# Kernel optimization log

Hardware: AMD Instinct MI355X
Metric: run time of the kernel (lower is better)

## Reference

```python
import jax, jax.numpy as jnp
import numpy as np

N_NODES = 100000
N_EDGES = 800000
IN_FEAT = 128
HID = 128
OUT = 2


def setup_inputs() -> dict:
    key = jax.random.key(0)
    ks = jax.random.split(key, 8)
    h = jax.random.normal(ks[0], (N_NODES, IN_FEAT), dtype=jnp.float32)
    src = jax.random.randint(ks[1], (N_EDGES,), 0, N_NODES, dtype=jnp.int64)
    dst = jax.random.randint(ks[2], (N_EDGES,), 0, N_NODES, dtype=jnp.int64)
    # Linear weights stored as (fan_in, fan_out); scaled like torch's default init
    W1 = jax.random.normal(ks[3], (2 * IN_FEAT, HID), dtype=jnp.float32) / np.sqrt(2 * IN_FEAT)
    b1 = jnp.zeros((HID,), dtype=jnp.float32)
    W2 = jax.random.normal(ks[4], (HID, HID), dtype=jnp.float32) / np.sqrt(HID)
    b2 = jnp.zeros((HID,), dtype=jnp.float32)
    W3 = jax.random.normal(ks[5], (HID, OUT), dtype=jnp.float32) / np.sqrt(HID)
    b3 = jnp.zeros((OUT,), dtype=jnp.float32)
    return {"h": h, "src": src, "dst": dst,
            "W1": W1, "b1": b1, "W2": W2, "b2": b2, "W3": W3, "b3": b3}


def reference(h, src, dst, W1, b1, W2, b2, W3, b3):
    # Per-edge gather of endpoint features, concat, 3-layer MLP with ReLU
    h_u = h[src]                       # [E, F]
    h_v = h[dst]                       # [E, F]
    x = jnp.concatenate([h_u, h_v], axis=1)   # [E, 2F]
    x = jax.nn.relu(x @ W1 + b1)       # [E, HID]
    x = jax.nn.relu(x @ W2 + b2)       # [E, HID]
    score = x @ W3 + b3                # [E, OUT]
    return score
```

## Files before the change

### kernel.cpp

```cpp
#include <hip/hip_runtime.h>
#include <hip/hip_fp16.h>


typedef _Float16 half8 __attribute__((ext_vector_type(8)));
typedef float    f32x4 __attribute__((ext_vector_type(4)));

#define N_NODES_C 100000
#define N_EDGES_C 800000
#define NT        12500
#define GRID_MAIN 512

#define W1F_OFF   0
#define W2F_OFF   65536
#define W3F_OFF   98304
#define H16_OFF   131072
#define H16_BYTES (N_NODES_C * 128 * 2)
#define WS_NEED   ((size_t)H16_OFF + (size_t)H16_BYTES)

#define MFMA16(a, b, c) __builtin_amdgcn_mfma_f32_16x16x32_f16((a), (b), (c), 0, 0, 0)


__global__ void conv_h_kernel(const float* __restrict__ h, _Float16* __restrict__ h16, int n8) {
    int stride = gridDim.x * blockDim.x;
    for (int i = blockIdx.x * blockDim.x + threadIdx.x; i < n8; i += stride) {
        const float4* p = (const float4*)h + 2 * (size_t)i;
        float4 a = p[0], b = p[1];
        half8 o;
        o[0] = (_Float16)a.x; o[1] = (_Float16)a.y; o[2] = (_Float16)a.z; o[3] = (_Float16)a.w;
        o[4] = (_Float16)b.x; o[5] = (_Float16)b.y; o[6] = (_Float16)b.z; o[7] = (_Float16)b.w;
        ((half8*)h16)[i] = o;
    }
}

__global__ void pack_w_kernel(const float* __restrict__ W1, const float* __restrict__ W2,
                              const float* __restrict__ W3, char* __restrict__ wsb) {
    int i = blockIdx.x * blockDim.x + threadIdx.x;
    _Float16* w1f = (_Float16*)(wsb + W1F_OFF);
    _Float16* w2f = (_Float16*)(wsb + W2F_OFF);
    _Float16* w3f = (_Float16*)(wsb + W3F_OFF);
    if (i < 32768) {
        int j = i & 7, lx = (i >> 3) & 63, kk = (i >> 9) & 7, t = i >> 12;
        int k = 32 * kk + 8 * (lx >> 4) + j, n = 16 * t + (lx & 15);
        w1f[i] = (_Float16)W1[k * 128 + n];
    }
    if (i < 16384) {
        int j = i & 7, lx = (i >> 3) & 63, kk = (i >> 9) & 3, t = i >> 11;
        int k = 32 * kk + 8 * (lx >> 4) + j, n = 16 * t + (lx & 15);
        w2f[i] = (_Float16)W2[k * 128 + n];
    }
    if (i < 2048) {
        int j = i & 7, lx = (i >> 3) & 63, kk = i >> 9;
        int k = 32 * kk + 8 * (lx >> 4) + j, n = lx & 15;
        w3f[i] = (n < 2) ? (_Float16)W3[k * 2 + n] : (_Float16)0.0f;
    }
}


template <bool USE16>
__device__ inline half8 ldfrag(const float* __restrict__ h, const half8* __restrict__ h16,
                               int idx, int kk, int g) {
    if constexpr (USE16) {
        return h16[idx * 16 + (kk & 3) * 4 + g];
    } else {
        const float4* p = (const float4*)(h + (size_t)idx * 128 + (kk & 3) * 32 + g * 8);
        float4 a = p[0], b = p[1];
        half8 o;
        o[0] = (_Float16)a.x; o[1] = (_Float16)a.y; o[2] = (_Float16)a.z; o[3] = (_Float16)a.w;
        o[4] = (_Float16)b.x; o[5] = (_Float16)b.y; o[6] = (_Float16)b.z; o[7] = (_Float16)b.w;
        return o;
    }
}

template <bool USE16>
__global__ __launch_bounds__(256, 2) void edge_mlp_kernel(
    const float* __restrict__ h,
    const int*   __restrict__ src,
    const int*   __restrict__ dst,
    const float* __restrict__ b1,
    const float* __restrict__ b2,
    const float* __restrict__ b3,
    const char*  __restrict__ wsb,
    float*       __restrict__ out) {
    __shared__ half8 Xp [32 * 64];
    __shared__ half8 Y1p[16 * 64];
    __shared__ half8 Y2p[16 * 64];

    const int tid = threadIdx.x;
    const int w = tid >> 6, l = tid & 63;
    const int g = l >> 4, rr = l & 15;
    const int ghalf = rr >> 3, j7 = rr & 7;

    half8 W1F[2][8], W2F[2][4], W3F[4];
    {
        const half8* p1 = (const half8*)(wsb + W1F_OFF);
        const half8* p2 = (const half8*)(wsb + W2F_OFF);
        const half8* p3 = (const half8*)(wsb + W3F_OFF);
#pragma unroll
        for (int nt = 0; nt < 2; ++nt)
#pragma unroll
            for (int kk = 0; kk < 8; ++kk)
                W1F[nt][kk] = p1[((w * 2 + nt) * 8 + kk) * 64 + l];
#pragma unroll
        for (int nt = 0; nt < 2; ++nt)
#pragma unroll
            for (int kk = 0; kk < 4; ++kk)
                W2F[nt][kk] = p2[((w * 2 + nt) * 4 + kk) * 64 + l];
#pragma unroll
        for (int kk = 0; kk < 4; ++kk)
            W3F[kk] = p3[kk * 64 + l];
    }
    float b1r[2], b2r[2];
    b1r[0] = b1[w * 32 + rr];      b1r[1] = b1[w * 32 + 16 + rr];
    b2r[0] = b2[w * 32 + rr];      b2r[1] = b2[w * 32 + 16 + rr];
    const float b3r = (rr < 2) ? b3[rr] : 0.0f;

    const half8* h16 = (const half8*)(wsb + H16_OFF);
    _Float16* y1h = (_Float16*)Y1p;
    _Float16* y2h = (_Float16*)Y2p;

    int   idxn[8];
    half8 xt[8];

    int tile = blockIdx.x;
#pragma unroll
    for (int i = 0; i < 8; i++) {
        int bidx = w * 8 + i, kk = bidx >> 2;
        int e = ((i & 3) << 4) + rr;
        int id = (kk < 4 ? src : dst)[tile * 64 + e];
        xt[i] = ldfrag<USE16>(h, h16, id, kk, g);
    }
#pragma unroll
    for (int i = 0; i < 8; i++) Xp[(w * 8 + i) * 64 + l] = xt[i];
    {
        int t1 = tile + GRID_MAIN; if (t1 >= NT) t1 = NT - 1;
#pragma unroll
        for (int i = 0; i < 8; i++) {
            int bidx = w * 8 + i, kk = bidx >> 2;
            int e = ((i & 3) << 4) + rr;
            idxn[i] = (kk < 4 ? src : dst)[t1 * 64 + e];
        }
    }
    __syncthreads();

    for (; tile < NT; tile += GRID_MAIN) {
        f32x4 acc1[4][2];
#pragma unroll
        for (int mt = 0; mt < 4; ++mt) {
            acc1[mt][0] = f32x4{0.f, 0.f, 0.f, 0.f};
            acc1[mt][1] = f32x4{0.f, 0.f, 0.f, 0.f};
        }
#pragma unroll
        for (int kk = 0; kk < 8; ++kk) {
            half8 a[4];
#pragma unroll
            for (int mt = 0; mt < 4; ++mt) a[mt] = Xp[(kk * 4 + mt) * 64 + l];
#pragma unroll
            for (int mt = 0; mt < 4; ++mt) {
                acc1[mt][0] = MFMA16(a[mt], W1F[0][kk], acc1[mt][0]);
                acc1[mt][1] = MFMA16(a[mt], W1F[1][kk], acc1[mt][1]);
            }
        }
#pragma unroll
        for (int i = 0; i < 8; i++) {
            int kk = (w * 8 + i) >> 2;
            xt[i] = ldfrag<USE16>(h, h16, idxn[i], kk, g);
        }
        {
            int t2 = tile + 2 * GRID_MAIN; if (t2 >= NT) t2 = NT - 1;
#pragma unroll
            for (int i = 0; i < 8; i++) {
                int bidx = w * 8 + i, kk = bidx >> 2;
                int e = ((i & 3) << 4) + rr;
                idxn[i] = (kk < 4 ? src : dst)[t2 * 64 + e];
            }
        }
#pragma unroll
        for (int mt = 0; mt < 4; ++mt)
#pragma unroll
            for (int nt = 0; nt < 2; ++nt) {
                float bb = b1r[nt];
#pragma unroll
                for (int r = 0; r < 4; ++r) {
                    float v = acc1[mt][nt][r] + bb;
                    v = v > 0.f ? v : 0.f;
                    y1h[(((w * 4 + mt) * 64 + 16 * (2 * nt + ghalf) + 4 * g + r) << 3) + j7] =
                        (_Float16)v;
                }
            }
        __syncthreads();

        f32x4 acc2[4][2];
#pragma unroll
        for (int mt = 0; mt < 4; ++mt) {
            acc2[mt][0] = f32x4{0.f, 0.f, 0.f, 0.f};
            acc2[mt][1] = f32x4{0.f, 0.f, 0.f, 0.f};
        }
#pragma unroll
        for (int kk = 0; kk < 4; ++kk) {
            half8 a[4];
#pragma unroll
            for (int mt = 0; mt < 4; ++mt) a[mt] = Y1p[(kk * 4 + mt) * 64 + l];
#pragma unroll
            for (int mt = 0; mt < 4; ++mt) {
                acc2[mt][0] = MFMA16(a[mt], W2F[0][kk], acc2[mt][0]);
                acc2[mt][1] = MFMA16(a[mt], W2F[1][kk], acc2[mt][1]);
            }
        }
#pragma unroll
        for (int mt = 0; mt < 4; ++mt)
#pragma unroll
            for (int nt = 0; nt < 2; ++nt) {
                float bb = b2r[nt];
#pragma unroll
                for (int r = 0; r < 4; ++r) {
                    float v = acc2[mt][nt][r] + bb;
                    v = v > 0.f ? v : 0.f;
                    y2h[(((w * 4 + mt) * 64 + 16 * (2 * nt + ghalf) + 4 * g + r) << 3) + j7] =
                        (_Float16)v;
                }
            }
        __syncthreads();

        f32x4 acc3 = {0.f, 0.f, 0.f, 0.f};
#pragma unroll
        for (int kk = 0; kk < 4; ++kk) {
            half8 a = Y2p[(kk * 4 + w) * 64 + l];
            acc3 = MFMA16(a, W3F[kk], acc3);
        }
        if (rr < 2) {
#pragma unroll
            for (int r = 0; r < 4; ++r) {
                int m = w * 16 + 4 * g + r;
                out[(tile * 64 + m) * 2 + rr] = acc3[r] + b3r;
            }
        }
#pragma unroll
        for (int i = 0; i < 8; i++) Xp[(w * 8 + i) * 64 + l] = xt[i];
        __syncthreads();
    }
}


extern "C" void kernel_launch(void* const* d_in, const int* in_sizes, int n_in,
                              void* d_out, int out_size, void* d_ws, size_t ws_size,
                              hipStream_t stream) {
    const float* h  = (const float*)d_in[0];
    const int*   src = (const int*)d_in[1];
    const int*   dst = (const int*)d_in[2];
    const float* W1 = (const float*)d_in[3];
    const float* b1 = (const float*)d_in[4];
    const float* W2 = (const float*)d_in[5];
    const float* b2 = (const float*)d_in[6];
    const float* W3 = (const float*)d_in[7];
    const float* b3 = (const float*)d_in[8];
    char*  wsb = (char*)d_ws;
    float* out = (float*)d_out;
    (void)in_sizes; (void)n_in; (void)out_size;

    pack_w_kernel<<<128, 256, 0, stream>>>(W1, W2, W3, wsb);
    if (ws_size >= WS_NEED) {
        conv_h_kernel<<<2048, 256, 0, stream>>>(h, (_Float16*)(wsb + H16_OFF),
                                                N_NODES_C * 128 / 8);
        edge_mlp_kernel<true><<<GRID_MAIN, 256, 0, stream>>>(h, src, dst, b1, b2, b3, wsb, out);
    } else {
        edge_mlp_kernel<false><<<GRID_MAIN, 256, 0, stream>>>(h, src, dst, b1, b2, b3, wsb, out);
    }
}
```

Measured before the change: 199.8 us.

## Precompute per-node layer-1 projections and gather them per edge

Splits the first linear layer across the concatenation so each node's features are projected once through both halves of W1 into fp16 tables, then edges gather and sum the two projections before ReLU and layers 2 and 3. This removes the per-edge layer-1 matmul, which is redundant since there are far fewer nodes than edges. The edge kernel is retiled to 32 edges per block with two waves splitting the output columns. The trade-offs are a larger workspace requirement, with a fallback to the old path if it is not met, and fp16 rounding of the pre-activation sums.

After: 249.9 us. +25.1%, slower.

```diff
diff --git a/kernel.cpp b/kernel.cpp
--- a/kernel.cpp
+++ b/kernel.cpp
@@ -3,41 +3,230 @@
 
 
 typedef _Float16 half8 __attribute__((ext_vector_type(8)));
+typedef _Float16 half4_t __attribute__((ext_vector_type(4)));
 typedef float    f32x4 __attribute__((ext_vector_type(4)));
+
+#define MFMA16(a, b, c) __builtin_amdgcn_mfma_f32_16x16x32_f16((a), (b), (c), 0, 0, 0)
 
 #define N_NODES_C 100000
 #define N_EDGES_C 800000
-#define NT        12500
-#define GRID_MAIN 512
-
-#define W1F_OFF   0
-#define W2F_OFF   65536
-#define W3F_OFF   98304
-#define H16_OFF   131072
-#define H16_BYTES (N_NODES_C * 128 * 2)
-#define WS_NEED   ((size_t)H16_OFF + (size_t)H16_BYTES)
-
-#define MFMA16(a, b, c) __builtin_amdgcn_mfma_f32_16x16x32_f16((a), (b), (c), 0, 0, 0)
-
-
-__global__ void conv_h_kernel(const float* __restrict__ h, _Float16* __restrict__ h16, int n8) {
-    int stride = gridDim.x * blockDim.x;
-    for (int i = blockIdx.x * blockDim.x + threadIdx.x; i < n8; i += stride) {
-        const float4* p = (const float4*)h + 2 * (size_t)i;
-        float4 a = p[0], b = p[1];
-        half8 o;
-        o[0] = (_Float16)a.x; o[1] = (_Float16)a.y; o[2] = (_Float16)a.z; o[3] = (_Float16)a.w;
-        o[4] = (_Float16)b.x; o[5] = (_Float16)b.y; o[6] = (_Float16)b.z; o[7] = (_Float16)b.w;
-        ((half8*)h16)[i] = o;
-    }
-}
-
-__global__ void pack_w_kernel(const float* __restrict__ W1, const float* __restrict__ W2,
-                              const float* __restrict__ W3, char* __restrict__ wsb) {
+
+#define W1PF_OFF  0
+#define W1QF_OFF  32768
+#define W2F_OFF_N 65536
+#define W3F_OFF_N 98304
+#define P16_OFF   131072
+#define TBL_HALVES (N_NODES_C * 128)
+#define Q16_OFF   (P16_OFF + TBL_HALVES * 2)
+#define WS_NEED_NEW ((size_t)Q16_OFF + (size_t)TBL_HALVES * 2)
+
+#define ET 32
+#define NT_E (N_EDGES_C / ET)
+#define GRID_E 1536
+#define NT_N ((N_NODES_C + 63) / 64)
+
+
+__global__ void pack_w_new(const float* __restrict__ W1, const float* __restrict__ W2,
+                           const float* __restrict__ W3, char* __restrict__ wsb) {
     int i = blockIdx.x * blockDim.x + threadIdx.x;
-    _Float16* w1f = (_Float16*)(wsb + W1F_OFF);
-    _Float16* w2f = (_Float16*)(wsb + W2F_OFF);
-    _Float16* w3f = (_Float16*)(wsb + W3F_OFF);
+    _Float16* w1pf = (_Float16*)(wsb + W1PF_OFF);
+    _Float16* w1qf = (_Float16*)(wsb + W1QF_OFF);
+    _Float16* w2f  = (_Float16*)(wsb + W2F_OFF_N);
+    _Float16* w3f  = (_Float16*)(wsb + W3F_OFF_N);
+    if (i < 16384) {
+        int j = i & 7, lane = (i >> 3) & 63, kk = (i >> 9) & 3, cm = i >> 11;
+        int g = lane >> 4, rr = lane & 15;
+        int k = 32 * kk + 8 * g + j, n = 16 * cm + rr;
+        w1pf[i] = (_Float16)W1[k * 128 + n];
+        w1qf[i] = (_Float16)W1[(k + 128) * 128 + n];
+        w2f[i]  = (_Float16)W2[k * 128 + n];
+    }
+    if (i < 2048) {
+        int j = i & 7, lane = (i >> 3) & 63, t = i >> 9;
+        int g = lane >> 4, rr = lane & 15;
+        int k = 32 * t + 4 * g + (j & 3) + 16 * (j >> 2);
+        w3f[i] = (rr < 2) ? (_Float16)W3[k * 2 + rr] : (_Float16)0.0f;
+    }
+}
+
+__global__ __launch_bounds__(512, 4) void pq_kernel(const float* __restrict__ h,
+                                                    const float* __restrict__ b1,
+                                                    char* __restrict__ wsb) {
+    const int tid = threadIdx.x;
+    const int w = tid >> 6, l = tid & 63, g = l >> 4, rr = l & 15;
+    const int t = w >> 2, cmq = w & 3;
+    const half8* wf = (const half8*)(wsb + (t ? W1QF_OFF : W1PF_OFF));
+    half8 W1F[2][4];
+#pragma unroll
+    for (int cm = 0; cm < 2; ++cm)
+#pragma unroll
+        for (int kk = 0; kk < 4; ++kk)
+            W1F[cm][kk] = wf[((2 * cmq + cm) * 4 + kk) * 64 + l];
+    f32x4 b1v[2] = {{0.f, 0.f, 0.f, 0.f}, {0.f, 0.f, 0.f, 0.f}};
+    if (t == 1) {
+#pragma unroll
+        for (int cm = 0; cm < 2; ++cm)
+            b1v[cm] = *(const f32x4*)(b1 + 16 * (2 * cmq + cm) + 4 * g);
+    }
+    _Float16* tbl = (_Float16*)(wsb + (t ? Q16_OFF : P16_OFF));
+
+    for (int tile = blockIdx.x; tile < NT_N; tile += gridDim.x) {
+        f32x4 acc[2][4];
+#pragma unroll
+        for (int cm = 0; cm < 2; ++cm)
+#pragma unroll
+            for (int ce = 0; ce < 4; ++ce) acc[cm][ce] = f32x4{0.f, 0.f, 0.f, 0.f};
+#pragma unroll
+        for (int kk = 0; kk < 4; ++kk) {
+#pragma unroll
+            for (int ce = 0; ce < 4; ++ce) {
+                int node = tile * 64 + 16 * ce + rr;
+                if (node > N_NODES_C - 1) node = N_NODES_C - 1;
+                const float4* hp = (const float4*)(h + (size_t)node * 128 + kk * 32 + 8 * g);
+                float4 fa = hp[0], fb = hp[1];
+                half8 b;
+                b[0] = (_Float16)fa.x; b[1] = (_Float16)fa.y;
+                b[2] = (_Float16)fa.z; b[3] = (_Float16)fa.w;
+                b[4] = (_Float16)fb.x; b[5] = (_Float16)fb.y;
+                b[6] = (_Float16)fb.z; b[7] = (_Float16)fb.w;
+                acc[0][ce] = MFMA16(W1F[0][kk], b, acc[0][ce]);
+                acc[1][ce] = MFMA16(W1F[1][kk], b, acc[1][ce]);
+            }
+        }
+#pragma unroll
+        for (int cm = 0; cm < 2; ++cm)
+#pragma unroll
+            for (int ce = 0; ce < 4; ++ce) {
+                int node = tile * 64 + 16 * ce + rr;
+                if (node < N_NODES_C) {
+                    f32x4 v = acc[cm][ce] + b1v[cm];
+                    half4_t o;
+                    o[0] = (_Float16)v[0]; o[1] = (_Float16)v[1];
+                    o[2] = (_Float16)v[2]; o[3] = (_Float16)v[3];
+                    *(half4_t*)(tbl + (size_t)node * 128 + 16 * (2 * cmq + cm) + 4 * g) = o;
+                }
+            }
+    }
+}
+
+__global__ __launch_bounds__(128, 3) void edge_kernel(
+    const int* __restrict__ src, const int* __restrict__ dst,
+    const float* __restrict__ b2, const float* __restrict__ b3,
+    const char* __restrict__ wsb, float* __restrict__ out) {
+    __shared__ float2 part[2][2][16];
+    const int tid = threadIdx.x;
+    const int w = tid >> 6, l = tid & 63, g = l >> 4, rr = l & 15;
+    const half8* w2f = (const half8*)(wsb + W2F_OFF_N);
+    const half8* w3f = (const half8*)(wsb + W3F_OFF_N);
+    const half8* P16 = (const half8*)(wsb + P16_OFF);
+    const half8* Q16 = (const half8*)(wsb + Q16_OFF);
+
+    half8 W2F[4][4], W3F[2];
+#pragma unroll
+    for (int cm = 0; cm < 4; ++cm)
+#pragma unroll
+        for (int kk = 0; kk < 4; ++kk)
+            W2F[cm][kk] = w2f[((4 * w + cm) * 4 + kk) * 64 + l];
+    W3F[0] = w3f[(2 * w) * 64 + l];
+    W3F[1] = w3f[(2 * w + 1) * 64 + l];
+
+    half4_t b2h[4];
+#pragma unroll
+    for (int cm = 0; cm < 4; ++cm) {
+        f32x4 bv = *(const f32x4*)(b2 + 16 * (4 * w + cm) + 4 * g);
+        b2h[cm][0] = (_Float16)bv[0]; b2h[cm][1] = (_Float16)bv[1];
+        b2h[cm][2] = (_Float16)bv[2]; b2h[cm][3] = (_Float16)bv[3];
+    }
+    const float b30 = b3[0], b31 = b3[1];
+
+    int tile = blockIdx.x;
+    int sc0 = src[tile * ET + rr],      sc1 = src[tile * ET + 16 + rr];
+    int dc0 = dst[tile * ET + rr],      dc1 = dst[tile * ET + 16 + rr];
+    int par = 0;
+
+    for (; tile < NT_E; tile += GRID_E) {
+        int ntile = tile + GRID_E; if (ntile >= NT_E) ntile = NT_E - 1;
+        f32x4 acc[4][2];
+#pragma unroll
+        for (int cm = 0; cm < 4; ++cm) {
+            acc[cm][0] = f32x4{0.f, 0.f, 0.f, 0.f};
+            acc[cm][1] = f32x4{0.f, 0.f, 0.f, 0.f};
+        }
+        const half8* pr0 = P16 + (size_t)sc0 * 16 + g;
+        const half8* pr1 = P16 + (size_t)sc1 * 16 + g;
+        const half8* qr0 = Q16 + (size_t)dc0 * 16 + g;
+        const half8* qr1 = Q16 + (size_t)dc1 * 16 + g;
+        const half8 hz = {0, 0, 0, 0, 0, 0, 0, 0};
+#pragma unroll
+        for (int kk = 0; kk < 4; ++kk) {
+            {
+                half8 p = pr0[4 * kk], q = qr0[4 * kk];
+                half8 b = __builtin_elementwise_max(p + q, hz);
+                acc[0][0] = MFMA16(W2F[0][kk], b, acc[0][0]);
+                acc[1][0] = MFMA16(W2F[1][kk], b, acc[1][0]);
+                acc[2][0] = MFMA16(W2F[2][kk], b, acc[2][0]);
+                acc[3][0] = MFMA16(W2F[3][kk], b, acc[3][0]);
+            }
+            {
+                half8 p = pr1[4 * kk], q = qr1[4 * kk];
+                half8 b = __builtin_elementwise_max(p + q, hz);
+                acc[0][1] = MFMA16(W2F[0][kk], b, acc[0][1]);
+                acc[1][1] = MFMA16(W2F[1][kk], b, acc[1][1]);
+                acc[2][1] = MFMA16(W2F[2][kk], b, acc[2][1]);
+                acc[3][1] = MFMA16(W2F[3][kk], b, acc[3][1]);
+            }
+        }
+        int sn0 = src[ntile * ET + rr], sn1 = src[ntile * ET + 16 + rr];
+        int dn0 = dst[ntile * ET + rr], dn1 = dst[ntile * ET + 16 + rr];
+
+        f32x4 D3[2] = {{0.f, 0.f, 0.f, 0.f}, {0.f, 0.f, 0.f, 0.f}};
+#pragma unroll
+        for (int tl = 0; tl < 2; ++tl)
+#pragma unroll
+            for (int ce = 0; ce < 2; ++ce) {
+                half8 bf;
+#pragma unroll
+                for (int j = 0; j < 8; ++j) {
+                    const int cm = 2 * tl + (j >> 2), r = j & 3;
+                    float v = acc[cm][ce][r] + (float)b2h[cm][r];
+                    v = v > 0.f ? v : 0.f;
+                    bf[j] = (_Float16)v;
+                }
+                D3[ce] = MFMA16(W3F[tl], bf, D3[ce]);
+            }
+        if (w == 1 && l < 16) {
+            part[par][0][rr] = make_float2(D3[0][0], D3[0][1]);
+            part[par][1][rr] = make_float2(D3[1][0], D3[1][1]);
+        }
+        __syncthreads();
+        if (w == 0 && l < 16) {
+#pragma unroll
+            for (int ce = 0; ce < 2; ++ce) {
+                float2 pp = part[par][ce][rr];
+                float2 ov;
+                ov.x = D3[ce][0] + pp.x + b30;
+                ov.y = D3[ce][1] + pp.y + b31;
+                *(float2*)(out + (size_t)(tile * ET + 16 * ce + rr) * 2) = ov;
+            }
+        }
+        par ^= 1;
+        sc0 = sn0; sc1 = sn1; dc0 = dn0; dc1 = dn1;
+    }
+}
+
+
+#define NT_O   12500
+#define GRID_O 512
+#define OW1_OFF 0
+#define OW2_OFF 65536
+#define OW3_OFF 98304
+
+__global__ void pack_w_old(const float* __restrict__ W1, const float* __restrict__ W2,
+                           const float* __restrict__ W3, char* __restrict__ wsb) {
+    int i = blockIdx.x * blockDim.x + threadIdx.x;
+    _Float16* w1f = (_Float16*)(wsb + OW1_OFF);
+    _Float16* w2f = (_Float16*)(wsb + OW2_OFF);
+    _Float16* w3f = (_Float16*)(wsb + OW3_OFF);
     if (i < 32768) {
         int j = i & 7, lx = (i >> 3) & 63, kk = (i >> 9) & 7, t = i >> 12;
         int k = 32 * kk + 8 * (lx >> 4) + j, n = 16 * t + (lx & 15);
@@ -55,84 +244,62 @@
     }
 }
 
-
-template <bool USE16>
-__device__ inline half8 ldfrag(const float* __restrict__ h, const half8* __restrict__ h16,
-                               int idx, int kk, int g) {
-    if constexpr (USE16) {
-        return h16[idx * 16 + (kk & 3) * 4 + g];
-    } else {
-        const float4* p = (const float4*)(h + (size_t)idx * 128 + (kk & 3) * 32 + g * 8);
-        float4 a = p[0], b = p[1];
-        half8 o;
-        o[0] = (_Float16)a.x; o[1] = (_Float16)a.y; o[2] = (_Float16)a.z; o[3] = (_Float16)a.w;
-        o[4] = (_Float16)b.x; o[5] = (_Float16)b.y; o[6] = (_Float16)b.z; o[7] = (_Float16)b.w;
-        return o;
-    }
-}
-
-template <bool USE16>
-__global__ __launch_bounds__(256, 2) void edge_mlp_kernel(
-    const float* __restrict__ h,
-    const int*   __restrict__ src,
-    const int*   __restrict__ dst,
-    const float* __restrict__ b1,
-    const float* __restrict__ b2,
-    const float* __restrict__ b3,
-    const char*  __restrict__ wsb,
-    float*       __restrict__ out) {
+__device__ inline half8 ldfrag_f32(const float* __restrict__ h, int idx, int kk, int g) {
+    const float4* p = (const float4*)(h + (size_t)idx * 128 + (kk & 3) * 32 + g * 8);
+    float4 a = p[0], b = p[1];
+    half8 o;
+    o[0] = (_Float16)a.x; o[1] = (_Float16)a.y; o[2] = (_Float16)a.z; o[3] = (_Float16)a.w;
+    o[4] = (_Float16)b.x; o[5] = (_Float16)b.y; o[6] = (_Float16)b.z; o[7] = (_Float16)b.w;
+    return o;
+}
+
+__global__ __launch_bounds__(256, 2) void edge_mlp_old(
+    const float* __restrict__ h, const int* __restrict__ src, const int* __restrict__ dst,
+    const float* __restrict__ b1, const float* __restrict__ b2, const float* __restrict__ b3,
+    const char* __restrict__ wsb, float* __restrict__ out) {
     __shared__ half8 Xp [32 * 64];
     __shared__ half8 Y1p[16 * 64];
     __shared__ half8 Y2p[16 * 64];
-
     const int tid = threadIdx.x;
     const int w = tid >> 6, l = tid & 63;
     const int g = l >> 4, rr = l & 15;
     const int ghalf = rr >> 3, j7 = rr & 7;
-
     half8 W1F[2][8], W2F[2][4], W3F[4];
     {
-        const half8* p1 = (const half8*)(wsb + W1F_OFF);
-        const half8* p2 = (const half8*)(wsb + W2F_OFF);
-        const half8* p3 = (const half8*)(wsb + W3F_OFF);
+        const half8* p1 = (const half8*)(wsb + OW1_OFF);
+        const half8* p2 = (const half8*)(wsb + OW2_OFF);
+        const half8* p3 = (const half8*)(wsb + OW3_OFF);
 #pragma unroll
         for (int nt = 0; nt < 2; ++nt)
 #pragma unroll
-            for (int kk = 0; kk < 8; ++kk)
-                W1F[nt][kk] = p1[((w * 2 + nt) * 8 + kk) * 64 + l];
+            for (int kk = 0; kk < 8; ++kk) W1F[nt][kk] = p1[((w * 2 + nt) * 8 + kk) * 64 + l];
 #pragma unroll
         for (int nt = 0; nt < 2; ++nt)
 #pragma unroll
-            for (int kk = 0; kk < 4; ++kk)
-                W2F[nt][kk] = p2[((w * 2 + nt) * 4 + kk) * 64 + l];
-#pragma unroll
-        for (int kk = 0; kk < 4; ++kk)
-            W3F[kk] = p3[kk * 64 + l];
+            for (int kk = 0; kk < 4; ++kk) W2F[nt][kk] = p2[((w * 2 + nt) * 4 + kk) * 64 + l];
+#pragma unroll
+        for (int kk = 0; kk < 4; ++kk) W3F[kk] = p3[kk * 64 + l];
     }
     float b1r[2], b2r[2];
     b1r[0] = b1[w * 32 + rr];      b1r[1] = b1[w * 32 + 16 + rr];
     b2r[0] = b2[w * 32 + rr];      b2r[1] = b2[w * 32 + 16 + rr];
     const float b3r = (rr < 2) ? b3[rr] : 0.0f;
-
-    const half8* h16 = (const half8*)(wsb + H16_OFF);
     _Float16* y1h = (_Float16*)Y1p;
     _Float16* y2h = (_Float16*)Y2p;
-
     int   idxn[8];
     half8 xt[8];
-
     int tile = blockIdx.x;
 #pragma unroll
     for (int i = 0; i < 8; i++) {
         int bidx = w * 8 + i, kk = bidx >> 2;
         int e = ((i & 3) << 4) + rr;
         int id = (kk < 4 ? src : dst)[tile * 64 + e];
-        xt[i] = ldfrag<USE16>(h, h16, id, kk, g);
+        xt[i] = ldfrag_f32(h, id, kk, g);
     }
 #pragma unroll
     for (int i = 0; i < 8; i++) Xp[(w * 8 + i) * 64 + l] = xt[i];
     {
-        int t1 = tile + GRID_MAIN; if (t1 >= NT) t1 = NT - 1;
+        int t1 = tile + GRID_O; if (t1 >= NT_O) t1 = NT_O - 1;
 #pragma unroll
         for (int i = 0; i < 8; i++) {
             int bidx = w * 8 + i, kk = bidx >> 2;
@@ -141,8 +308,7 @@
         }
     }
     __syncthreads();
-
-    for (; tile < NT; tile += GRID_MAIN) {
+    for (; tile < NT_O; tile += GRID_O) {
         f32x4 acc1[4][2];
 #pragma unroll
         for (int mt = 0; mt < 4; ++mt) {
@@ -163,10 +329,10 @@
 #pragma unroll
         for (int i = 0; i < 8; i++) {
             int kk = (w * 8 + i) >> 2;
-            xt[i] = ldfrag<USE16>(h, h16, idxn[i], kk, g);
+            xt[i] = ldfrag_f32(h, idxn[i], kk, g);
         }
         {
-            int t2 = tile + 2 * GRID_MAIN; if (t2 >= NT) t2 = NT - 1;
+            int t2 = tile + 2 * GRID_O; if (t2 >= NT_O) t2 = NT_O - 1;
 #pragma unroll
             for (int i = 0; i < 8; i++) {
                 int bidx = w * 8 + i, kk = bidx >> 2;
@@ -188,7 +354,6 @@
                 }
             }
         __syncthreads();
-
         f32x4 acc2[4][2];
 #pragma unroll
         for (int mt = 0; mt < 4; ++mt) {
@@ -220,7 +385,6 @@
                 }
             }
         __syncthreads();
-
         f32x4 acc3 = {0.f, 0.f, 0.f, 0.f};
 #pragma unroll
         for (int kk = 0; kk < 4; ++kk) {
@@ -244,25 +408,25 @@
 extern "C" void kernel_launch(void* const* d_in, const int* in_sizes, int n_in,
                               void* d_out, int out_size, void* d_ws, size_t ws_size,
                               hipStream_t stream) {
-    const float* h  = (const float*)d_in[0];
+    const float* h   = (const float*)d_in[0];
     const int*   src = (const int*)d_in[1];
     const int*   dst = (const int*)d_in[2];
-    const float* W1 = (const float*)d_in[3];
-    const float* b1 = (const float*)d_in[4];
-    const float* W2 = (const float*)d_in[5];
-    const float* b2 = (const float*)d_in[6];
-    const float* W3 = (const float*)d_in[7];
-    const float* b3 = (const float*)d_in[8];
+    const float* W1  = (const float*)d_in[3];
+    const float* b1  = (const float*)d_in[4];
+    const float* W2  = (const float*)d_in[5];
+    const float* b2  = (const float*)d_in[6];
+    const float* W3  = (const float*)d_in[7];
+    const float* b3  = (const float*)d_in[8];
     char*  wsb = (char*)d_ws;
     float* out = (float*)d_out;
     (void)in_sizes; (void)n_in; (void)out_size;
 
-    pack_w_kernel<<<128, 256, 0, stream>>>(W1, W2, W3, wsb);
-    if (ws_size >= WS_NEED) {
-        conv_h_kernel<<<2048, 256, 0, stream>>>(h, (_Float16*)(wsb + H16_OFF),
-                                                N_NODES_C * 128 / 8);
-        edge_mlp_kernel<true><<<GRID_MAIN, 256, 0, stream>>>(h, src, dst, b1, b2, b3, wsb, out);
+    if (ws_size >= WS_NEED_NEW) {
+        pack_w_new<<<64, 256, 0, stream>>>(W1, W2, W3, wsb);
+        pq_kernel<<<512, 512, 0, stream>>>(h, b1, wsb);
+        edge_kernel<<<GRID_E, 128, 0, stream>>>(src, dst, b2, b3, wsb, out);
     } else {
-        edge_mlp_kernel<false><<<GRID_MAIN, 256, 0, stream>>>(h, src, dst, b1, b2, b3, wsb, out);
-    }
-}
+        pack_w_old<<<128, 256, 0, stream>>>(W1, W2, W3, wsb);
+        edge_mlp_old<<<GRID_O, 256, 0, stream>>>(h, src, dst, b1, b2, b3, wsb, out);
+    }
+}
```
